# Kernel optimization log

Hardware: AMD Instinct MI355X
Metric: run time of the kernel (lower is better)

The kernel has to match this reference:

```python
import jax, jax.numpy as jnp
import numpy as np

N, E = 2048, 65536
EMBED, H0, H1 = 64, 128, 128
VOCAB = 625  # 5**k with k=4
SLOPE = 0.01  # F.leaky_relu_ default negative slope


def setup_inputs() -> dict:
    key = jax.random.key(0)
    ks = jax.random.split(key, 20)
    f = jax.random.normal
    return {
        "node_ids": jax.random.randint(ks[0], (N,), 0, VOCAB),
        "edge_index": jax.random.randint(ks[1], (2, E), 0, N),
        "edge_attr": jax.random.uniform(ks[2], (E, 1), dtype=jnp.float32),
        "m": (jax.random.uniform(ks[3], (N, N)) > 0.5).astype(jnp.float32),
        "emb": f(ks[4], (VOCAB, EMBED), dtype=jnp.float32) * 0.1,
        "l0_lin1": f(ks[5], (H0, EMBED + 1), dtype=jnp.float32) * 0.1,
        "l0_lin2": f(ks[6], (H0, H0), dtype=jnp.float32) * 0.1,
        "l0_att_l": f(ks[7], (H0,), dtype=jnp.float32) * 0.1,
        "l0_att_r": f(ks[8], (EMBED,), dtype=jnp.float32) * 0.1,
        "l0_bias": f(ks[9], (H0,), dtype=jnp.float32) * 0.1,
        "l1_lin1": f(ks[10], (H1, H0 + 1), dtype=jnp.float32) * 0.1,
        "l1_lin2": f(ks[11], (H1, H1), dtype=jnp.float32) * 0.1,
        "l1_att_l": f(ks[12], (H1,), dtype=jnp.float32) * 0.1,
        "l1_att_r": f(ks[13], (H0,), dtype=jnp.float32) * 0.1,
        "l1_bias": f(ks[14], (H1,), dtype=jnp.float32) * 0.1,
        "W1": f(ks[15], (20, (EMBED + H0 + H1) * 2), dtype=jnp.float32) * 0.1,
        "b1": f(ks[16], (20,), dtype=jnp.float32) * 0.1,
        "W2": f(ks[17], (20,), dtype=jnp.float32) * 0.1,
        "b2": f(ks[18], (1,), dtype=jnp.float32) * 0.1,
    }


def _segment_softmax(alpha, index, n):
    # numerically-stable softmax over edges grouped by destination node
    amax = jax.ops.segment_max(alpha, index, num_segments=n)
    amax = jnp.where(jnp.isfinite(amax), amax, 0.0)
    e = jnp.exp(alpha - amax[index])
    denom = jax.ops.segment_sum(e, index, num_segments=n)
    return e / (denom[index] + 1e-16)


def _gate_conv(x, src, dst, edge_attr, lin1, lin2, att_l, att_r, bias, n):
    # PyG AttentiveFP GATEConv: message = lin2(leaky_relu(lin1([x_j, e]))) * alpha
    h = jax.nn.leaky_relu(jnp.concatenate([x[src], edge_attr], axis=-1) @ lin1.T, SLOPE)  # [E,out]
    alpha = jax.nn.leaky_relu(h @ att_l + x[dst] @ att_r, SLOPE)  # [E]
    alpha = _segment_softmax(alpha, dst, n)
    msg = (h @ lin2.T) * alpha[:, None]
    return jax.ops.segment_sum(msg, dst, num_segments=n) + bias


def reference(node_ids, edge_index, edge_attr, m, emb,
              l0_lin1, l0_lin2, l0_att_l, l0_att_r, l0_bias,
              l1_lin1, l1_lin2, l1_att_l, l1_att_r, l1_bias,
              W1, b1, W2, b2):
    src, dst = edge_index[0], edge_index[1]
    x = emb[node_ids]  # [N, EMBED]
    h1 = jax.nn.relu(_gate_conv(x, src, dst, edge_attr, l0_lin1, l0_lin2, l0_att_l, l0_att_r, l0_bias, N))
    h2 = jax.nn.relu(_gate_conv(h1, src, dst, edge_attr, l1_lin1, l1_lin2, l1_att_l, l1_att_r, l1_bias, N))
    feat = jnp.concatenate([x, h1, h2], axis=-1)  # [N, C], C = EMBED+H0+H1
    C = feat.shape[-1]
    # 1x1 conv over concat([x_i, x_j]) == split linear: out[c,i,j] = W1[c,:C]@feat[i] + W1[c,C:]@feat[j] + b1[c]
    a = feat @ W1[:, :C].T  # [N, 20] row (i) term
    b = feat @ W1[:, C:].T  # [N, 20] col (j) term
    h = jax.nn.relu(a[:, None, :] + b[None, :, :] + b1)  # [N, N, 20]
    logits = (h @ W2 + b2[0]) * m  # [N, N]; mask multiplies logits as in original
    return jax.nn.softmax(logits, axis=1)
```

## Files before the change

### kernel.cpp

```cpp
#include <hip/hip_runtime.h>
#include <math.h>

#define N 2048
#define E 65536
#define EMBED 64
#define H 128
#define NT 20
#define C3 320
#define CAP 96
#define SLOPE 0.01f
#define NBLK 256
#define NTHR 512

__device__ __forceinline__ float leaky(float x) { return x > 0.f ? x : SLOPE * x; }

__device__ __forceinline__ float wave_sum(float v) {
#pragma unroll
    for (int o = 32; o > 0; o >>= 1) v += __shfl_xor(v, o, 64);
    return v;
}

__device__ __forceinline__ void grid_sync(int* bar, int target) {
    __syncthreads();
    if (threadIdx.x == 0) {
        __builtin_amdgcn_fence(__ATOMIC_RELEASE, "agent");
        __hip_atomic_fetch_add(bar, 1, __ATOMIC_RELAXED, __HIP_MEMORY_SCOPE_AGENT);
        while (__hip_atomic_load(bar, __ATOMIC_RELAXED, __HIP_MEMORY_SCOPE_AGENT) < target)
            __builtin_amdgcn_s_sleep(2);
        __builtin_amdgcn_fence(__ATOMIC_ACQUIRE, "agent");
    }
    __syncthreads();
}

__device__ __forceinline__ void gate_wave(
    int dst, int lane, float xr,
    const float* __restrict__ A,
    float w0, float w1, float attl0, float attl1,
    const int* __restrict__ srcs, const float* __restrict__ eas, int cnt,
    float& out0, float& out1) {
    int c0 = 2 * lane;
    int base = dst * CAP;
    float mmax = -INFINITY, s = 0.f, v0 = 0.f, v1 = 0.f;
    for (int i0 = 0; i0 < cnt; i0 += 8) {
        int nb = cnt - i0; if (nb > 8) nb = 8;
        float h0[8], h1v[8], p[8];
#pragma unroll
        for (int e = 0; e < 8; e++) {
            float ea = 0.f; float2 av = make_float2(0.f, 0.f);
            if (e < nb) {
                int sn = srcs[base + i0 + e];
                ea = eas[base + i0 + e];
                av = *(const float2*)&A[sn * H + c0];
            }
            h0[e] = leaky(fmaf(w0, ea, av.x));
            h1v[e] = leaky(fmaf(w1, ea, av.y));
            p[e] = h0[e] * attl0 + h1v[e] * attl1;
        }
#pragma unroll
        for (int o = 32; o > 0; o >>= 1) {
#pragma unroll
            for (int e = 0; e < 8; e++) p[e] += __shfl_xor(p[e], o, 64);
        }
        float alpha[8];
#pragma unroll
        for (int e = 0; e < 8; e++)
            alpha[e] = (e < nb) ? leaky(p[e] + xr) : -INFINITY;
        float mb = alpha[0];
#pragma unroll
        for (int e = 1; e < 8; e++) mb = fmaxf(mb, alpha[e]);
        float mnew = fmaxf(mmax, mb);
        float scale = __expf(mmax - mnew);
        float sw = 0.f, sv0 = 0.f, sv1 = 0.f;
#pragma unroll
        for (int e = 0; e < 8; e++) {
            float we = __expf(alpha[e] - mnew);
            sw += we;
            sv0 = fmaf(we, h0[e], sv0);
            sv1 = fmaf(we, h1v[e], sv1);
        }
        s = fmaf(s, scale, sw);
        v0 = fmaf(v0, scale, sv0);
        v1 = fmaf(v1, scale, sv1);
        mmax = mnew;
    }
    float inv = 1.f / (s + 1e-16f);
    out0 = v0 * inv;
    out1 = v1 * inv;
}

__global__ __launch_bounds__(NTHR) void k_fused(
    const int* __restrict__ ids, const int* __restrict__ ei,
    const float* __restrict__ eattr, const float* __restrict__ mmat,
    const float* __restrict__ emb,
    const float* __restrict__ l0_lin1, const float* __restrict__ l0_lin2,
    const float* __restrict__ l0_att_l, const float* __restrict__ l0_att_r,
    const float* __restrict__ l0_bias,
    const float* __restrict__ l1_lin1, const float* __restrict__ l1_lin2,
    const float* __restrict__ l1_att_l, const float* __restrict__ l1_att_r,
    const float* __restrict__ l1_bias,
    const float* __restrict__ W1, const float* __restrict__ b1,
    const float* __restrict__ W2, const float* __restrict__ b2,
    int* __restrict__ cursor, int* __restrict__ bar,
    int* __restrict__ srcs, float* __restrict__ eas,
    float* __restrict__ x, float* __restrict__ A0, float* __restrict__ A1,
    float* __restrict__ h1, float* __restrict__ aArr, float* __restrict__ bT,
    float* __restrict__ WT1, float* __restrict__ LT0, float* __restrict__ LT1,
    float* __restrict__ out) {
    __shared__ float smem[EMBED * 130];
    const int b = blockIdx.x;
    const int tid = threadIdx.x;
    const int gtid = b * NTHR + tid;

    if (gtid < E) {
        int d = ei[E + gtid];
        int pos = atomicAdd(&cursor[d], 1);
        if (pos < CAP) {
            srcs[d * CAP + pos] = ei[gtid];
            eas[d * CAP + pos] = eattr[gtid];
        }
    } else if (gtid < E + 16384) {
        int j = gtid - E;
        WT1[j] = l1_lin1[(j & 127) * (H + 1) + (j >> 7)];
    } else if (gtid < E + 32768) {
        int j = gtid - (E + 16384);
        LT0[j] = l0_lin2[(j & 127) * H + (j >> 7)];
    } else if (gtid < E + 49152) {
        int j = gtid - (E + 32768);
        LT1[j] = l1_lin2[(j & 127) * H + (j >> 7)];
    }
    {
        int g = gtid >> 6, c = gtid & 63;
        x[gtid] = emb[ids[g] * EMBED + c];
    }
    {
        float (*lw)[130] = (float(*)[130])smem;
        for (int j = tid; j < H * (EMBED + 1); j += NTHR) {
            int kk = j / (EMBED + 1), c = j % (EMBED + 1);
            float v = l0_lin1[j];
            if (c < EMBED) lw[c][kk] = v;
        }
        __syncthreads();
        int n0 = b * 8;
        int k = tid & 127, grp = tid >> 7;
        int nnA = __builtin_amdgcn_readfirstlane(n0 + grp);
        int nnB = __builtin_amdgcn_readfirstlane(n0 + grp + 4);
        const float* xrA = emb + (size_t)ids[nnA] * EMBED;
        const float* xrB = emb + (size_t)ids[nnB] * EMBED;
        float accA = 0.f, accB = 0.f;
#pragma unroll 4
        for (int c = 0; c < EMBED; c++) {
            float wt = lw[c][k];
            accA = fmaf(xrA[c], wt, accA);
            accB = fmaf(xrB[c], wt, accB);
        }
        A0[(n0 + grp) * H + k] = accA;
        A0[(n0 + grp + 4) * H + k] = accB;
    }
    grid_sync(bar, NBLK);

    {
        float (*agg_s)[H] = (float(*)[H])smem;
        float (*hs)[H] = (float(*)[H])(smem + 8 * H);
        int n0 = b * 8;
        int wv = __builtin_amdgcn_readfirstlane(tid >> 6);
        int lane = tid & 63;
        int c0 = 2 * lane;
        int dst = n0 + wv;
        float xr = wave_sum(x[dst * EMBED + lane] * l0_att_r[lane]);
        float attl0 = l0_att_l[c0], attl1 = l0_att_l[c0 + 1];
        float w0 = l0_lin1[c0 * (EMBED + 1) + EMBED];
        float w1 = l0_lin1[(c0 + 1) * (EMBED + 1) + EMBED];
        int cnt = cursor[dst]; if (cnt > CAP) cnt = CAP;

        float o0, o1;
        gate_wave(dst, lane, xr, A0, w0, w1, attl0, attl1, srcs, eas, cnt, o0, o1);
        agg_s[wv][c0] = o0;
        agg_s[wv][c0 + 1] = o1;
        __syncthreads();

        int k = tid & 127, q = tid >> 7;
        float bk = l0_bias[k];
        float acc0 = bk, acc1 = bk;
#pragma unroll 2
        for (int ct = 0; ct < H / 4; ct++) {
            float u0 = LT0[(4 * ct + 0) * H + k];
            float u1 = LT0[(4 * ct + 1) * H + k];
            float u2 = LT0[(4 * ct + 2) * H + k];
            float u3 = LT0[(4 * ct + 3) * H + k];
            float4 f0 = *(const float4*)&agg_s[q][4 * ct];
            float4 f1 = *(const float4*)&agg_s[q + 4][4 * ct];
            acc0 = fmaf(f0.x, u0, acc0); acc0 = fmaf(f0.y, u1, acc0);
            acc0 = fmaf(f0.z, u2, acc0); acc0 = fmaf(f0.w, u3, acc0);
            acc1 = fmaf(f1.x, u0, acc1); acc1 = fmaf(f1.y, u1, acc1);
            acc1 = fmaf(f1.z, u2, acc1); acc1 = fmaf(f1.w, u3, acc1);
        }
        float hv0 = fmaxf(acc0, 0.f), hv1 = fmaxf(acc1, 0.f);
        h1[(n0 + q) * H + k] = hv0;
        h1[(n0 + q + 4) * H + k] = hv1;
        hs[q][k] = hv0;
        hs[q + 4][k] = hv1;
        __syncthreads();

        float a0 = 0.f, a1 = 0.f;
#pragma unroll 2
        for (int ct = 0; ct < H / 4; ct++) {
            float u0 = WT1[(4 * ct + 0) * H + k];
            float u1 = WT1[(4 * ct + 1) * H + k];
            float u2 = WT1[(4 * ct + 2) * H + k];
            float u3 = WT1[(4 * ct + 3) * H + k];
            float4 f0 = *(const float4*)&hs[q][4 * ct];
            float4 f1 = *(const float4*)&hs[q + 4][4 * ct];
            a0 = fmaf(f0.x, u0, a0); a0 = fmaf(f0.y, u1, a0);
            a0 = fmaf(f0.z, u2, a0); a0 = fmaf(f0.w, u3, a0);
            a1 = fmaf(f1.x, u0, a1); a1 = fmaf(f1.y, u1, a1);
            a1 = fmaf(f1.z, u2, a1); a1 = fmaf(f1.w, u3, a1);
        }
        A1[(n0 + q) * H + k] = a0;
        A1[(n0 + q + 4) * H + k] = a1;
    }
    grid_sync(bar, 2 * NBLK);

    {
        float (*agg_s)[H] = (float(*)[H])smem;
        float (*feat)[C3] = (float(*)[C3])(smem + 8 * H);
        int n0 = b * 8;
        int wv = __builtin_amdgcn_readfirstlane(tid >> 6);
        int lane = tid & 63;
        int c0 = 2 * lane;
        int dst = n0 + wv;
        float xr = wave_sum(h1[dst * H + lane] * l1_att_r[lane] +
                            h1[dst * H + 64 + lane] * l1_att_r[64 + lane]);
        float attl0 = l1_att_l[c0], attl1 = l1_att_l[c0 + 1];
        float w0 = l1_lin1[c0 * (H + 1) + H];
        float w1 = l1_lin1[(c0 + 1) * (H + 1) + H];
        int cnt = cursor[dst]; if (cnt > CAP) cnt = CAP;

        float o0, o1;
        gate_wave(dst, lane, xr, A1, w0, w1, attl0, attl1, srcs, eas, cnt, o0, o1);
        agg_s[wv][c0] = o0;
        agg_s[wv][c0 + 1] = o1;

        for (int idx = tid; idx < 8 * EMBED; idx += NTHR) {
            int g = idx >> 6, c = idx & 63;
            feat[g][c] = x[(n0 + g) * EMBED + c];
        }
        for (int idx = tid; idx < 8 * H; idx += NTHR) {
            int g = idx >> 7, c = idx & 127;
            feat[g][EMBED + c] = h1[(n0 + g) * H + c];
        }
        __syncthreads();

        int k = tid & 127, q = tid >> 7;
        float bk = l1_bias[k];
        float acc0 = bk, acc1 = bk;
#pragma unroll 2
        for (int ct = 0; ct < H / 4; ct++) {
            float u0 = LT1[(4 * ct + 0) * H + k];
            float u1 = LT1[(4 * ct + 1) * H + k];
            float u2 = LT1[(4 * ct + 2) * H + k];
            float u3 = LT1[(4 * ct + 3) * H + k];
            float4 f0 = *(const float4*)&agg_s[q][4 * ct];
            float4 f1 = *(const float4*)&agg_s[q + 4][4 * ct];
            acc0 = fmaf(f0.x, u0, acc0); acc0 = fmaf(f0.y, u1, acc0);
            acc0 = fmaf(f0.z, u2, acc0); acc0 = fmaf(f0.w, u3, acc0);
            acc1 = fmaf(f1.x, u0, acc1); acc1 = fmaf(f1.y, u1, acc1);
            acc1 = fmaf(f1.z, u2, acc1); acc1 = fmaf(f1.w, u3, acc1);
        }
        feat[q][EMBED + H + k] = fmaxf(acc0, 0.f);
        feat[q + 4][EMBED + H + k] = fmaxf(acc1, 0.f);
        __syncthreads();

        if (tid < 320) {
            int g = tid / 40, u = tid % 40;
            int t = u % 20, side = u / 20;
            const float* wrow = W1 + t * (2 * C3) + side * C3;
            float s = 0.f;
#pragma unroll 4
            for (int ct = 0; ct < C3 / 4; ct++) {
                float4 fv = *(const float4*)&feat[g][4 * ct];
                float4 wv4 = *(const float4*)&wrow[4 * ct];
                s = fmaf(fv.x, wv4.x, s);
                s = fmaf(fv.y, wv4.y, s);
                s = fmaf(fv.z, wv4.z, s);
                s = fmaf(fv.w, wv4.w, s);
            }
            if (side == 0) aArr[(n0 + g) * NT + t] = s;
            else bT[t * N + (n0 + g)] = s;
        }
    }
    grid_sync(bar, 3 * NBLK);

    {
        float* red = smem + (tid >> 8) * 16;
        int t256 = tid & 255;
        int i0 = b * 8 + (tid >> 8) * 4;
        int lane = t256 & 63, wv = t256 >> 6;
        float w2r[NT];
#pragma unroll
        for (int t = 0; t < NT; t++) w2r[t] = W2[t];
        float b2v = b2[0];
        float ab[4][NT];
#pragma unroll
        for (int g = 0; g < 4; g++) {
#pragma unroll
            for (int t = 0; t < NT; t++)
                ab[g][t] = aArr[(i0 + g) * NT + t] + b1[t];
        }
        float l[4][8];
        float tmax[4] = {-INFINITY, -INFINITY, -INFINITY, -INFINITY};
#pragma unroll
        for (int it = 0; it < 8; it++) {
            int j = t256 + 256 * it;
            float bt[NT];
#pragma unroll
            for (int t = 0; t < NT; t++) bt[t] = bT[t * N + j];
#pragma unroll
            for (int g = 0; g < 4; g++) {
                float s = b2v;
#pragma unroll
                for (int t = 0; t < NT; t++)
                    s += fmaxf(ab[g][t] + bt[t], 0.f) * w2r[t];
                s *= mmat[(size_t)(i0 + g) * N + j];
                l[g][it] = s;
                tmax[g] = fmaxf(tmax[g], s);
            }
        }
#pragma unroll
        for (int g = 0; g < 4; g++) {
#pragma unroll
            for (int o = 32; o > 0; o >>= 1)
                tmax[g] = fmaxf(tmax[g], __shfl_xor(tmax[g], o, 64));
        }
        if (lane == 0) {
#pragma unroll
            for (int g = 0; g < 4; g++) red[wv * 4 + g] = tmax[g];
        }
        __syncthreads();
        float mfin[4];
#pragma unroll
        for (int g = 0; g < 4; g++)
            mfin[g] = fmaxf(fmaxf(red[g], red[4 + g]), fmaxf(red[8 + g], red[12 + g]));
        __syncthreads();

        float ts[4] = {0.f, 0.f, 0.f, 0.f};
#pragma unroll
        for (int it = 0; it < 8; it++) {
#pragma unroll
            for (int g = 0; g < 4; g++) {
                float e = __expf(l[g][it] - mfin[g]);
                l[g][it] = e;
                ts[g] += e;
            }
        }
#pragma unroll
        for (int g = 0; g < 4; g++) {
#pragma unroll
            for (int o = 32; o > 0; o >>= 1) ts[g] += __shfl_xor(ts[g], o, 64);
        }
        if (lane == 0) {
#pragma unroll
            for (int g = 0; g < 4; g++) red[wv * 4 + g] = ts[g];
        }
        __syncthreads();
        float inv[4];
#pragma unroll
        for (int g = 0; g < 4; g++)
            inv[g] = 1.f / (red[g] + red[4 + g] + red[8 + g] + red[12 + g]);

#pragma unroll
        for (int it = 0; it < 8; it++) {
            int j = t256 + 256 * it;
#pragma unroll
            for (int g = 0; g < 4; g++)
                out[(size_t)(i0 + g) * N + j] = l[g][it] * inv[g];
        }
    }
}

extern "C" void kernel_launch(void* const* d_in, const int* in_sizes, int n_in,
                              void* d_out, int out_size, void* d_ws, size_t ws_size,
                              hipStream_t stream) {
    const int*   node_ids = (const int*)d_in[0];
    const int*   ei       = (const int*)d_in[1];
    const float* eattr    = (const float*)d_in[2];
    const float* mmat     = (const float*)d_in[3];
    const float* emb      = (const float*)d_in[4];
    const float* l0_lin1  = (const float*)d_in[5];
    const float* l0_lin2  = (const float*)d_in[6];
    const float* l0_att_l = (const float*)d_in[7];
    const float* l0_att_r = (const float*)d_in[8];
    const float* l0_bias  = (const float*)d_in[9];
    const float* l1_lin1  = (const float*)d_in[10];
    const float* l1_lin2  = (const float*)d_in[11];
    const float* l1_att_l = (const float*)d_in[12];
    const float* l1_att_r = (const float*)d_in[13];
    const float* l1_bias  = (const float*)d_in[14];
    const float* W1       = (const float*)d_in[15];
    const float* b1       = (const float*)d_in[16];
    const float* W2       = (const float*)d_in[17];
    const float* b2       = (const float*)d_in[18];
    float* out = (float*)d_out;

    char* w = (char*)d_ws;
    auto alloc = [&](size_t bytes) {
        char* p = w;
        w += (bytes + 255) & ~(size_t)255;
        return p;
    };
    int*   cursor = (int*)alloc((N + 64) * sizeof(int));
    int*   bar    = cursor + N;
    int*   srcs   = (int*)alloc(N * CAP * sizeof(int));
    float* eas    = (float*)alloc(N * CAP * sizeof(float));
    float* x      = (float*)alloc(N * EMBED * sizeof(float));
    float* A0     = (float*)alloc(N * H * sizeof(float));
    float* A1     = (float*)alloc(N * H * sizeof(float));
    float* h1     = (float*)alloc(N * H * sizeof(float));
    float* aArr   = (float*)alloc(N * NT * sizeof(float));
    float* bT     = (float*)alloc(NT * N * sizeof(float));
    float* WT1    = (float*)alloc(H * H * sizeof(float));
    float* LT0    = (float*)alloc(H * H * sizeof(float));
    float* LT1    = (float*)alloc(H * H * sizeof(float));

    hipMemsetAsync(cursor, 0, (N + 64) * sizeof(int), stream);

    k_fused<<<NBLK, NTHR, 0, stream>>>(node_ids, ei, eattr, mmat, emb,
                                       l0_lin1, l0_lin2, l0_att_l, l0_att_r, l0_bias,
                                       l1_lin1, l1_lin2, l1_att_l, l1_att_r, l1_bias,
                                       W1, b1, W2, b2,
                                       cursor, bar, srcs, eas, x, A0, A1, h1,
                                       aArr, bT, WT1, LT0, LT1, out);
}
```

Before: 220.2 us.

## Keep per-block node data in LDS, pack edges, shard grid barrier, vectorize softmax

Packs edge source and attribute into one int2 array so each edge needs a single load, and processes 16 edges per step in the gate aggregation. Keeps x, h1 and the row term in shared memory instead of global buffers, since each block only needs its own 8 nodes. Splits the grid barrier counter across 8 cache-line-separated slots with a longer sleep to reduce atomic contention. Rewrites the final pairwise softmax so each block handles 8 full rows with float4 loads and stores, keeping the logits in LDS. This raises LDS use to about 88KB and register pressure, which may reduce occupancy.

```diff
diff --git a/kernel.cpp b/kernel.cpp
--- a/kernel.cpp
+++ b/kernel.cpp
@@ -20,37 +20,44 @@
     return v;
 }
 
-__device__ __forceinline__ void grid_sync(int* bar, int target) {
+__device__ __forceinline__ void grid_sync(int* ctr, int target, int b) {
     __syncthreads();
     if (threadIdx.x == 0) {
         __builtin_amdgcn_fence(__ATOMIC_RELEASE, "agent");
-        __hip_atomic_fetch_add(bar, 1, __ATOMIC_RELAXED, __HIP_MEMORY_SCOPE_AGENT);
-        while (__hip_atomic_load(bar, __ATOMIC_RELAXED, __HIP_MEMORY_SCOPE_AGENT) < target)
-            __builtin_amdgcn_s_sleep(2);
+        __hip_atomic_fetch_add(&ctr[(b & 7) << 6], 1, __ATOMIC_RELAXED,
+                               __HIP_MEMORY_SCOPE_AGENT);
+        for (;;) {
+            int sum = 0;
+#pragma unroll
+            for (int i = 0; i < 8; i++)
+                sum += __hip_atomic_load(&ctr[i << 6], __ATOMIC_RELAXED,
+                                         __HIP_MEMORY_SCOPE_AGENT);
+            if (sum >= target) break;
+            __builtin_amdgcn_s_sleep(32);
+        }
         __builtin_amdgcn_fence(__ATOMIC_ACQUIRE, "agent");
     }
     __syncthreads();
 }
 
-__device__ __forceinline__ void gate_wave(
-    int dst, int lane, float xr,
+__device__ __forceinline__ void gate_wave16(
+    int base, int lane, float xr,
     const float* __restrict__ A,
     float w0, float w1, float attl0, float attl1,
-    const int* __restrict__ srcs, const float* __restrict__ eas, int cnt,
+    const int2* __restrict__ se, int cnt,
     float& out0, float& out1) {
     int c0 = 2 * lane;
-    int base = dst * CAP;
     float mmax = -INFINITY, s = 0.f, v0 = 0.f, v1 = 0.f;
-    for (int i0 = 0; i0 < cnt; i0 += 8) {
-        int nb = cnt - i0; if (nb > 8) nb = 8;
-        float h0[8], h1v[8], p[8];
-#pragma unroll
-        for (int e = 0; e < 8; e++) {
+    for (int i0 = 0; i0 < cnt; i0 += 16) {
+        int nb = cnt - i0; if (nb > 16) nb = 16;
+        float h0[16], h1v[16], p[16];
+#pragma unroll
+        for (int e = 0; e < 16; e++) {
             float ea = 0.f; float2 av = make_float2(0.f, 0.f);
             if (e < nb) {
-                int sn = srcs[base + i0 + e];
-                ea = eas[base + i0 + e];
-                av = *(const float2*)&A[sn * H + c0];
+                int2 v = se[base + i0 + e];
+                ea = __int_as_float(v.y);
+                av = *(const float2*)&A[v.x * H + c0];
             }
             h0[e] = leaky(fmaf(w0, ea, av.x));
             h1v[e] = leaky(fmaf(w1, ea, av.y));
@@ -59,20 +66,20 @@
 #pragma unroll
         for (int o = 32; o > 0; o >>= 1) {
 #pragma unroll
-            for (int e = 0; e < 8; e++) p[e] += __shfl_xor(p[e], o, 64);
-        }
-        float alpha[8];
-#pragma unroll
-        for (int e = 0; e < 8; e++)
+            for (int e = 0; e < 16; e++) p[e] += __shfl_xor(p[e], o, 64);
+        }
+        float alpha[16];
+#pragma unroll
+        for (int e = 0; e < 16; e++)
             alpha[e] = (e < nb) ? leaky(p[e] + xr) : -INFINITY;
         float mb = alpha[0];
 #pragma unroll
-        for (int e = 1; e < 8; e++) mb = fmaxf(mb, alpha[e]);
+        for (int e = 1; e < 16; e++) mb = fmaxf(mb, alpha[e]);
         float mnew = fmaxf(mmax, mb);
         float scale = __expf(mmax - mnew);
         float sw = 0.f, sv0 = 0.f, sv1 = 0.f;
 #pragma unroll
-        for (int e = 0; e < 8; e++) {
+        for (int e = 0; e < 16; e++) {
             float we = __expf(alpha[e] - mnew);
             sw += we;
             sv0 = fmaf(we, h0[e], sv0);
@@ -101,81 +108,78 @@
     const float* __restrict__ W1, const float* __restrict__ b1,
     const float* __restrict__ W2, const float* __restrict__ b2,
     int* __restrict__ cursor, int* __restrict__ bar,
-    int* __restrict__ srcs, float* __restrict__ eas,
-    float* __restrict__ x, float* __restrict__ A0, float* __restrict__ A1,
-    float* __restrict__ h1, float* __restrict__ aArr, float* __restrict__ bT,
+    int2* __restrict__ se,
+    float* __restrict__ A0, float* __restrict__ A1,
+    float* __restrict__ bT,
     float* __restrict__ WT1, float* __restrict__ LT0, float* __restrict__ LT1,
     float* __restrict__ out) {
-    __shared__ float smem[EMBED * 130];
+    __shared__ float smem[512 + 1024 + 1024 + 2560 + 160 + 16384 + 64 + 64];
+    float* xL   = smem;
+    float* agg  = smem + 512;
+    float* hs   = smem + 1536;
+    float* feat = smem + 2560;
+    float* aL   = smem + 5120;
+    float* Lrow = smem + 5280;
+    float* redM = smem + 21664;
+    float* redS = smem + 21728;
     const int b = blockIdx.x;
     const int tid = threadIdx.x;
     const int gtid = b * NTHR + tid;
+    const int n0 = b * 8;
 
     if (gtid < E) {
         int d = ei[E + gtid];
         int pos = atomicAdd(&cursor[d], 1);
-        if (pos < CAP) {
-            srcs[d * CAP + pos] = ei[gtid];
-            eas[d * CAP + pos] = eattr[gtid];
-        }
-    } else if (gtid < E + 16384) {
+        if (pos < CAP)
+            se[d * CAP + pos] = make_int2(ei[gtid], __float_as_int(eattr[gtid]));
+    } else {
         int j = gtid - E;
-        WT1[j] = l1_lin1[(j & 127) * (H + 1) + (j >> 7)];
-    } else if (gtid < E + 32768) {
-        int j = gtid - (E + 16384);
-        LT0[j] = l0_lin2[(j & 127) * H + (j >> 7)];
-    } else if (gtid < E + 49152) {
-        int j = gtid - (E + 32768);
-        LT1[j] = l1_lin2[(j & 127) * H + (j >> 7)];
+        if (j < 16384) {
+            WT1[j] = l1_lin1[(j & 127) * (H + 1) + (j >> 7)];
+        } else if (j < 32768) {
+            int jj = j - 16384;
+            LT0[jj] = l0_lin2[(jj & 127) * H + (jj >> 7)];
+        } else if (j < 49152) {
+            int jj = j - 32768;
+            LT1[jj] = l1_lin2[(jj & 127) * H + (jj >> 7)];
+        }
     }
     {
-        int g = gtid >> 6, c = gtid & 63;
-        x[gtid] = emb[ids[g] * EMBED + c];
-    }
+        int g = tid >> 6, c = tid & 63;
+        xL[g * EMBED + c] = emb[ids[n0 + g] * EMBED + c];
+    }
+    __syncthreads();
     {
-        float (*lw)[130] = (float(*)[130])smem;
-        for (int j = tid; j < H * (EMBED + 1); j += NTHR) {
-            int kk = j / (EMBED + 1), c = j % (EMBED + 1);
-            float v = l0_lin1[j];
-            if (c < EMBED) lw[c][kk] = v;
-        }
-        __syncthreads();
-        int n0 = b * 8;
-        int k = tid & 127, grp = tid >> 7;
-        int nnA = __builtin_amdgcn_readfirstlane(n0 + grp);
-        int nnB = __builtin_amdgcn_readfirstlane(n0 + grp + 4);
-        const float* xrA = emb + (size_t)ids[nnA] * EMBED;
-        const float* xrB = emb + (size_t)ids[nnB] * EMBED;
+        int k = tid & 127, q = tid >> 7;
+        const float* wr = l0_lin1 + k * (EMBED + 1);
         float accA = 0.f, accB = 0.f;
 #pragma unroll 4
         for (int c = 0; c < EMBED; c++) {
-            float wt = lw[c][k];
-            accA = fmaf(xrA[c], wt, accA);
-            accB = fmaf(xrB[c], wt, accB);
-        }
-        A0[(n0 + grp) * H + k] = accA;
-        A0[(n0 + grp + 4) * H + k] = accB;
-    }
-    grid_sync(bar, NBLK);
+            float w = wr[c];
+            accA = fmaf(xL[q * EMBED + c], w, accA);
+            accB = fmaf(xL[(q + 4) * EMBED + c], w, accB);
+        }
+        A0[(n0 + q) * H + k] = accA;
+        A0[(n0 + q + 4) * H + k] = accB;
+    }
+    grid_sync(bar, NBLK, b);
 
     {
-        float (*agg_s)[H] = (float(*)[H])smem;
-        float (*hs)[H] = (float(*)[H])(smem + 8 * H);
-        int n0 = b * 8;
         int wv = __builtin_amdgcn_readfirstlane(tid >> 6);
         int lane = tid & 63;
         int c0 = 2 * lane;
         int dst = n0 + wv;
-        float xr = wave_sum(x[dst * EMBED + lane] * l0_att_r[lane]);
+
+        float xr = wave_sum(xL[wv * EMBED + lane] * l0_att_r[lane]);
         float attl0 = l0_att_l[c0], attl1 = l0_att_l[c0 + 1];
         float w0 = l0_lin1[c0 * (EMBED + 1) + EMBED];
         float w1 = l0_lin1[(c0 + 1) * (EMBED + 1) + EMBED];
         int cnt = cursor[dst]; if (cnt > CAP) cnt = CAP;
 
         float o0, o1;
-        gate_wave(dst, lane, xr, A0, w0, w1, attl0, attl1, srcs, eas, cnt, o0, o1);
-        agg_s[wv][c0] = o0;
-        agg_s[wv][c0 + 1] = o1;
+        gate_wave16(dst * CAP, lane, xr, A0, w0, w1, attl0, attl1, se, cnt, o0, o1);
+        agg[wv * H + c0] = o0;
+        agg[wv * H + c0 + 1] = o1;
         __syncthreads();
 
         int k = tid & 127, q = tid >> 7;
@@ -187,18 +191,15 @@
             float u1 = LT0[(4 * ct + 1) * H + k];
             float u2 = LT0[(4 * ct + 2) * H + k];
             float u3 = LT0[(4 * ct + 3) * H + k];
-            float4 f0 = *(const float4*)&agg_s[q][4 * ct];
-            float4 f1 = *(const float4*)&agg_s[q + 4][4 * ct];
+            float4 f0 = *(const float4*)&agg[q * H + 4 * ct];
+            float4 f1 = *(const float4*)&agg[(q + 4) * H + 4 * ct];
             acc0 = fmaf(f0.x, u0, acc0); acc0 = fmaf(f0.y, u1, acc0);
             acc0 = fmaf(f0.z, u2, acc0); acc0 = fmaf(f0.w, u3, acc0);
             acc1 = fmaf(f1.x, u0, acc1); acc1 = fmaf(f1.y, u1, acc1);
             acc1 = fmaf(f1.z, u2, acc1); acc1 = fmaf(f1.w, u3, acc1);
         }
-        float hv0 = fmaxf(acc0, 0.f), hv1 = fmaxf(acc1, 0.f);
-        h1[(n0 + q) * H + k] = hv0;
-        h1[(n0 + q + 4) * H + k] = hv1;
-        hs[q][k] = hv0;
-        hs[q + 4][k] = hv1;
+        hs[q * H + k] = fmaxf(acc0, 0.f);
+        hs[(q + 4) * H + k] = fmaxf(acc1, 0.f);
         __syncthreads();
 
         float a0 = 0.f, a1 = 0.f;
@@ -208,8 +209,8 @@
             float u1 = WT1[(4 * ct + 1) * H + k];
             float u2 = WT1[(4 * ct + 2) * H + k];
             float u3 = WT1[(4 * ct + 3) * H + k];
-            float4 f0 = *(const float4*)&hs[q][4 * ct];
-            float4 f1 = *(const float4*)&hs[q + 4][4 * ct];
+            float4 f0 = *(const float4*)&hs[q * H + 4 * ct];
+            float4 f1 = *(const float4*)&hs[(q + 4) * H + 4 * ct];
             a0 = fmaf(f0.x, u0, a0); a0 = fmaf(f0.y, u1, a0);
             a0 = fmaf(f0.z, u2, a0); a0 = fmaf(f0.w, u3, a0);
             a1 = fmaf(f1.x, u0, a1); a1 = fmaf(f1.y, u1, a1);
@@ -218,35 +219,33 @@
         A1[(n0 + q) * H + k] = a0;
         A1[(n0 + q + 4) * H + k] = a1;
     }
-    grid_sync(bar, 2 * NBLK);
+    grid_sync(bar, 2 * NBLK, b);
 
     {
-        float (*agg_s)[H] = (float(*)[H])smem;
-        float (*feat)[C3] = (float(*)[C3])(smem + 8 * H);
-        int n0 = b * 8;
         int wv = __builtin_amdgcn_readfirstlane(tid >> 6);
         int lane = tid & 63;
         int c0 = 2 * lane;
         int dst = n0 + wv;
-        float xr = wave_sum(h1[dst * H + lane] * l1_att_r[lane] +
-                            h1[dst * H + 64 + lane] * l1_att_r[64 + lane]);
+
+        float xr = wave_sum(hs[wv * H + lane] * l1_att_r[lane] +
+                            hs[wv * H + 64 + lane] * l1_att_r[64 + lane]);
         float attl0 = l1_att_l[c0], attl1 = l1_att_l[c0 + 1];
         float w0 = l1_lin1[c0 * (H + 1) + H];
         float w1 = l1_lin1[(c0 + 1) * (H + 1) + H];
         int cnt = cursor[dst]; if (cnt > CAP) cnt = CAP;
 
         float o0, o1;
-        gate_wave(dst, lane, xr, A1, w0, w1, attl0, attl1, srcs, eas, cnt, o0, o1);
-        agg_s[wv][c0] = o0;
-        agg_s[wv][c0 + 1] = o1;
+        gate_wave16(dst * CAP, lane, xr, A1, w0, w1, attl0, attl1, se, cnt, o0, o1);
+        agg[wv * H + c0] = o0;
+        agg[wv * H + c0 + 1] = o1;
 
         for (int idx = tid; idx < 8 * EMBED; idx += NTHR) {
             int g = idx >> 6, c = idx & 63;
-            feat[g][c] = x[(n0 + g) * EMBED + c];
+            feat[g * C3 + c] = xL[g * EMBED + c];
         }
         for (int idx = tid; idx < 8 * H; idx += NTHR) {
             int g = idx >> 7, c = idx & 127;
-            feat[g][EMBED + c] = h1[(n0 + g) * H + c];
+            feat[g * C3 + EMBED + c] = hs[g * H + c];
         }
         __syncthreads();
 
@@ -259,15 +258,15 @@
             float u1 = LT1[(4 * ct + 1) * H + k];
             float u2 = LT1[(4 * ct + 2) * H + k];
             float u3 = LT1[(4 * ct + 3) * H + k];
-            float4 f0 = *(const float4*)&agg_s[q][4 * ct];
-            float4 f1 = *(const float4*)&agg_s[q + 4][4 * ct];
+            float4 f0 = *(const float4*)&agg[q * H + 4 * ct];
+            float4 f1 = *(const float4*)&agg[(q + 4) * H + 4 * ct];
             acc0 = fmaf(f0.x, u0, acc0); acc0 = fmaf(f0.y, u1, acc0);
             acc0 = fmaf(f0.z, u2, acc0); acc0 = fmaf(f0.w, u3, acc0);
             acc1 = fmaf(f1.x, u0, acc1); acc1 = fmaf(f1.y, u1, acc1);
             acc1 = fmaf(f1.z, u2, acc1); acc1 = fmaf(f1.w, u3, acc1);
         }
-        feat[q][EMBED + H + k] = fmaxf(acc0, 0.f);
-        feat[q + 4][EMBED + H + k] = fmaxf(acc1, 0.f);
+        feat[q * C3 + EMBED + H + k] = fmaxf(acc0, 0.f);
+        feat[(q + 4) * C3 + EMBED + H + k] = fmaxf(acc1, 0.f);
         __syncthreads();
 
         if (tid < 320) {
@@ -277,102 +276,82 @@
             float s = 0.f;
 #pragma unroll 4
             for (int ct = 0; ct < C3 / 4; ct++) {
-                float4 fv = *(const float4*)&feat[g][4 * ct];
+                float4 fv = *(const float4*)&feat[g * C3 + 4 * ct];
                 float4 wv4 = *(const float4*)&wrow[4 * ct];
                 s = fmaf(fv.x, wv4.x, s);
                 s = fmaf(fv.y, wv4.y, s);
                 s = fmaf(fv.z, wv4.z, s);
                 s = fmaf(fv.w, wv4.w, s);
             }
-            if (side == 0) aArr[(n0 + g) * NT + t] = s;
+            if (side == 0) aL[g * NT + t] = s + b1[t];
             else bT[t * N + (n0 + g)] = s;
         }
     }
-    grid_sync(bar, 3 * NBLK);
+    grid_sync(bar, 3 * NBLK, b);
 
     {
-        float* red = smem + (tid >> 8) * 16;
-        int t256 = tid & 255;
-        int i0 = b * 8 + (tid >> 8) * 4;
-        int lane = t256 & 63, wv = t256 >> 6;
+        int lane = tid & 63, wv = tid >> 6;
+        int j = 4 * tid;
         float w2r[NT];
 #pragma unroll
         for (int t = 0; t < NT; t++) w2r[t] = W2[t];
         float b2v = b2[0];
-        float ab[4][NT];
-#pragma unroll
-        for (int g = 0; g < 4; g++) {
-#pragma unroll
-            for (int t = 0; t < NT; t++)
-                ab[g][t] = aArr[(i0 + g) * NT + t] + b1[t];
-        }
-        float l[4][8];
-        float tmax[4] = {-INFINITY, -INFINITY, -INFINITY, -INFINITY};
-#pragma unroll
-        for (int it = 0; it < 8; it++) {
-            int j = t256 + 256 * it;
-            float bt[NT];
-#pragma unroll
-            for (int t = 0; t < NT; t++) bt[t] = bT[t * N + j];
-#pragma unroll
-            for (int g = 0; g < 4; g++) {
-                float s = b2v;
-#pragma unroll
-                for (int t = 0; t < NT; t++)
-                    s += fmaxf(ab[g][t] + bt[t], 0.f) * w2r[t];
-                s *= mmat[(size_t)(i0 + g) * N + j];
-                l[g][it] = s;
-                tmax[g] = fmaxf(tmax[g], s);
+        float4 bt4[NT];
+#pragma unroll
+        for (int t = 0; t < NT; t++) bt4[t] = *(const float4*)&bT[t * N + j];
+
+#pragma unroll
+        for (int g = 0; g < 8; g++) {
+            float4 s4 = make_float4(b2v, b2v, b2v, b2v);
+#pragma unroll
+            for (int t = 0; t < NT; t++) {
+                float a = aL[g * NT + t];
+                float w = w2r[t];
+                s4.x = fmaf(fmaxf(a + bt4[t].x, 0.f), w, s4.x);
+                s4.y = fmaf(fmaxf(a + bt4[t].y, 0.f), w, s4.y);
+                s4.z = fmaf(fmaxf(a + bt4[t].z, 0.f), w, s4.z);
+                s4.w = fmaf(fmaxf(a + bt4[t].w, 0.f), w, s4.w);
             }
-        }
-#pragma unroll
-        for (int g = 0; g < 4; g++) {
-#pragma unroll
-            for (int o = 32; o > 0; o >>= 1)
-                tmax[g] = fmaxf(tmax[g], __shfl_xor(tmax[g], o, 64));
-        }
-        if (lane == 0) {
-#pragma unroll
-            for (int g = 0; g < 4; g++) red[wv * 4 + g] = tmax[g];
-        }
-        __syncthreads();
-        float mfin[4];
-#pragma unroll
-        for (int g = 0; g < 4; g++)
-            mfin[g] = fmaxf(fmaxf(red[g], red[4 + g]), fmaxf(red[8 + g], red[12 + g]));
-        __syncthreads();
-
-        float ts[4] = {0.f, 0.f, 0.f, 0.f};
-#pragma unroll
-        for (int it = 0; it < 8; it++) {
-#pragma unroll
-            for (int g = 0; g < 4; g++) {
-                float e = __expf(l[g][it] - mfin[g]);
-                l[g][it] = e;
-                ts[g] += e;
-            }
-        }
-#pragma unroll
-        for (int g = 0; g < 4; g++) {
-#pragma unroll
-            for (int o = 32; o > 0; o >>= 1) ts[g] += __shfl_xor(ts[g], o, 64);
-        }
-        if (lane == 0) {
-#pragma unroll
-            for (int g = 0; g < 4; g++) red[wv * 4 + g] = ts[g];
-        }
-        __syncthreads();
-        float inv[4];
-#pragma unroll
-        for (int g = 0; g < 4; g++)
-            inv[g] = 1.f / (red[g] + red[4 + g] + red[8 + g] + red[12 + g]);
-
-#pragma unroll
-        for (int it = 0; it < 8; it++) {
-            int j = t256 + 256 * it;
-#pragma unroll
-            for (int g = 0; g < 4; g++)
-                out[(size_t)(i0 + g) * N + j] = l[g][it] * inv[g];
+            float4 mm = *(const float4*)&mmat[(size_t)(n0 + g) * N + j];
+            s4.x *= mm.x; s4.y *= mm.y; s4.z *= mm.z; s4.w *= mm.w;
+            *(float4*)&Lrow[g * 2048 + j] = s4;
+            float tm = fmaxf(fmaxf(s4.x, s4.y), fmaxf(s4.z, s4.w));
+#pragma unroll
+            for (int o = 32; o > 0; o >>= 1) tm = fmaxf(tm, __shfl_xor(tm, o, 64));
+            if (lane == 0) redM[g * 8 + wv] = tm;
+        }
+        __syncthreads();
+        float mfin[8];
+#pragma unroll
+        for (int g = 0; g < 8; g++) {
+            float m = redM[g * 8 + 0];
+#pragma unroll
+            for (int w = 1; w < 8; w++) m = fmaxf(m, redM[g * 8 + w]);
+            mfin[g] = m;
+        }
+#pragma unroll
+        for (int g = 0; g < 8; g++) {
+            float4 v = *(const float4*)&Lrow[g * 2048 + j];
+            float ts = __expf(v.x - mfin[g]) + __expf(v.y - mfin[g]) +
+                       __expf(v.z - mfin[g]) + __expf(v.w - mfin[g]);
+#pragma unroll
+            for (int o = 32; o > 0; o >>= 1) ts += __shfl_xor(ts, o, 64);
+            if (lane == 0) redS[g * 8 + wv] = ts;
+        }
+        __syncthreads();
+#pragma unroll
+        for (int g = 0; g < 8; g++) {
+            float s = 0.f;
+#pragma unroll
+            for (int w = 0; w < 8; w++) s += redS[g * 8 + w];
+            float inv = 1.f / s;
+            float4 v = *(const float4*)&Lrow[g * 2048 + j];
+            float4 o4;
+            o4.x = __expf(v.x - mfin[g]) * inv;
+            o4.y = __expf(v.y - mfin[g]) * inv;
+            o4.z = __expf(v.z - mfin[g]) * inv;
+            o4.w = __expf(v.w - mfin[g]) * inv;
+            *(float4*)&out[(size_t)(n0 + g) * N + j] = o4;
         }
     }
 }
@@ -407,26 +386,22 @@
         w += (bytes + 255) & ~(size_t)255;
         return p;
     };
-    int*   cursor = (int*)alloc((N + 64) * sizeof(int));
+    int*   cursor = (int*)alloc((N + 512) * sizeof(int));
     int*   bar    = cursor + N;
-    int*   srcs   = (int*)alloc(N * CAP * sizeof(int));
-    float* eas    = (float*)alloc(N * CAP * sizeof(float));
-    float* x      = (float*)alloc(N * EMBED * sizeof(float));
+    int2*  se     = (int2*)alloc(N * CAP * sizeof(int2));
     float* A0     = (float*)alloc(N * H * sizeof(float));
     float* A1     = (float*)alloc(N * H * sizeof(float));
-    float* h1     = (float*)alloc(N * H * sizeof(float));
-    float* aArr   = (float*)alloc(N * NT * sizeof(float));
     float* bT     = (float*)alloc(NT * N * sizeof(float));
     float* WT1    = (float*)alloc(H * H * sizeof(float));
     float* LT0    = (float*)alloc(H * H * sizeof(float));
     float* LT1    = (float*)alloc(H * H * sizeof(float));
 
-    hipMemsetAsync(cursor, 0, (N + 64) * sizeof(int), stream);
+    hipMemsetAsync(cursor, 0, (N + 512) * sizeof(int), stream);
 
     k_fused<<<NBLK, NTHR, 0, stream>>>(node_ids, ei, eattr, mmat, emb,
                                        l0_lin1, l0_lin2, l0_att_l, l0_att_r, l0_bias,
                                        l1_lin1, l1_lin2, l1_att_l, l1_att_r, l1_bias,
                                        W1, b1, W2, b2,
-                                       cursor, bar, srcs, eas, x, A0, A1, h1,
-                                       aArr, bT, WT1, LT0, LT1, out);
+                                       cursor, bar, se, A0, A1,
+                                       bT, WT1, LT0, LT1, out);
 }
```

Result: faster. 204.9 us (-7.0%).
